# Kernel optimization log

Hardware: AMD Instinct MI355X
Metric: run time of the kernel (lower is better)

The kernel has to match this reference:

```python
import jax, jax.numpy as jnp
import numpy as np

B, N, IN, H, I, A, NA, NH = 4096, 8, 256, 256, 64, 64, 32, 256
VAR_FLOOR = 0.002
BN_EPS = 1e-5


def _lin(x, w, b):
    # torch Linear: x @ w.T + b, w: [out, in]
    return x @ w.T + b


def _bn_train(x, g, b):
    # BatchNorm1d in training mode: batch stats, biased variance
    mu = jnp.mean(x, axis=0)
    var = jnp.var(x, axis=0)
    return (x - mu) * jax.lax.rsqrt(var + BN_EPS) * g + b


def _intent_net(h_la, w1, b1, g, bbn, w2, b2):
    z = _lin(h_la, w1, b1)
    z = _bn_train(z, g, bbn)
    z = jax.nn.leaky_relu(z, 0.01)
    return _lin(z, w2, b2)


def setup_inputs() -> dict:
    key = jax.random.key(0)
    ks = jax.random.split(key, 30)
    s = 0.05
    d = {
        "inputs": jax.random.normal(ks[0], (B * N, IN), jnp.float32),
        "last_actions": jax.random.normal(ks[1], (B, N, NA), jnp.float32),
        "hidden_state": jax.random.normal(ks[2], (B * N, H), jnp.float32),
        "eps": jax.random.normal(ks[3], (B * N, I), jnp.float32),
        # fc1
        "fc1_w": jax.random.normal(ks[4], (H, IN), jnp.float32) * s,
        "fc1_b": jnp.zeros((H,), jnp.float32),
        # GRUCell (r,z,n gate order, torch layout)
        "gru_w_ih": jax.random.normal(ks[5], (3 * H, H), jnp.float32) * s,
        "gru_w_hh": jax.random.normal(ks[6], (3 * H, H), jnp.float32) * s,
        "gru_b_ih": jnp.zeros((3 * H,), jnp.float32),
        "gru_b_hh": jnp.zeros((3 * H,), jnp.float32),
        # intent_net: Linear(H+NA, NH) -> BN -> LeakyReLU -> Linear(NH, 2*I)
        "in1_w": jax.random.normal(ks[7], (NH, H + NA), jnp.float32) * s,
        "in1_b": jnp.zeros((NH,), jnp.float32),
        "bn_g": jnp.ones((NH,), jnp.float32),
        "bn_b": jnp.zeros((NH,), jnp.float32),
        "in2_w": jax.random.normal(ks[8], (2 * I, NH), jnp.float32) * s,
        "in2_b": jnp.zeros((2 * I,), jnp.float32),
        # attention projections
        "wq_w": jax.random.normal(ks[9], (A, I), jnp.float32) * s,
        "wq_b": jnp.zeros((A,), jnp.float32),
        "wk_w": jax.random.normal(ks[10], (A, I), jnp.float32) * s,
        "wk_b": jnp.zeros((A,), jnp.float32),
        "wv_w": jax.random.normal(ks[11], (A, I + H), jnp.float32) * s,
        "wv_b": jnp.zeros((A,), jnp.float32),
        # fc2
        "fc2_w": jax.random.normal(ks[12], (NA, H + A), jnp.float32) * s,
        "fc2_b": jnp.zeros((NA,), jnp.float32),
        "bs": B,
        "t": 1,
    }
    return d


def reference(inputs, last_actions, hidden_state, eps,
              fc1_w, fc1_b, gru_w_ih, gru_w_hh, gru_b_ih, gru_b_hh,
              in1_w, in1_b, bn_g, bn_b, in2_w, in2_b,
              wq_w, wq_b, wk_w, wk_b, wv_w, wv_b, fc2_w, fc2_b,
              bs, t):
    n = N
    x = jax.nn.relu(_lin(inputs, fc1_w, fc1_b))  # [bs*n, H]
    h_in = hidden_state.reshape(-1, H)
    # torch GRUCell
    gi = x @ gru_w_ih.T + gru_b_ih
    gh = h_in @ gru_w_hh.T + gru_b_hh
    i_r, i_z, i_n = jnp.split(gi, 3, axis=-1)
    h_r, h_z, h_n = jnp.split(gh, 3, axis=-1)
    r = jax.nn.sigmoid(i_r + h_r)
    z = jax.nn.sigmoid(i_z + h_z)
    nng = jnp.tanh(i_n + r * h_n)
    h = (1.0 - z) * nng + z * h_in  # [bs*n, H]

    la = last_actions.reshape(bs * n, NA)
    h_la = jnp.concatenate([h, la], axis=-1)
    ip = _intent_net(h_la, in1_w, in1_b, bn_g, bn_b, in2_w, in2_b)  # [bs*n, 2I]
    mean = ip[:, :I]
    std = jnp.maximum(jnp.exp(ip[:, I:]), VAR_FLOOR)
    intent = mean + eps * std  # reparameterized sample, [bs*n, I]

    q = _lin(intent, wq_w, wq_b).reshape(bs, n, A)  # query per agent i
    k = _lin(intent, wk_w, wk_b).reshape(bs, n, A)  # key per agent j
    scale = 1.0 / jnp.sqrt(jnp.float32(A))
    alpha = jnp.einsum('bia,bja->bij', q * scale, k)  # [bs, n, n]
    diag = jnp.eye(n, dtype=bool)
    alpha = jnp.where(diag[None], -1e9, alpha)
    alpha = jax.nn.softmax(alpha, axis=-1)

    v = _lin(jnp.concatenate([intent, h], axis=-1), wv_w, wv_b).reshape(bs, n, A)
    combined = jnp.einsum('bij,bja->bia', alpha, v).reshape(bs * n, A)

    local_Q = _lin(jnp.concatenate([h, combined], axis=-1), fc2_w, fc2_b).reshape(bs, n, NA)
    # final intent_embed: fresh intent_net output (no clamp/exp applied)
    intent_embed = _intent_net(h_la, in1_w, in1_b, bn_g, bn_b, in2_w, in2_b)
    return local_Q, h, intent, intent_embed
```

## Files before the change

### kernel.cpp

```cpp
#include <hip/hip_runtime.h>
#include <hip/hip_bf16.h>

#define BN_ 32768

using bf16 = __hip_bfloat16;
typedef __bf16 v8bf __attribute__((ext_vector_type(8)));
typedef unsigned short v8us __attribute__((ext_vector_type(8)));
typedef float v4f __attribute__((ext_vector_type(4)));

__device__ __forceinline__ float b2f(bf16 x) { return __bfloat162float(x); }
__device__ __forceinline__ bf16 f2b(float x) { return __float2bfloat16(x); }
__device__ __forceinline__ unsigned short f2bu(float x) {
  bf16 h = __float2bfloat16(x);
  return *reinterpret_cast<unsigned short*>(&h);
}
__device__ __forceinline__ float bu2f(unsigned short u) {
  union { unsigned int i; float f; } x;
  x.i = ((unsigned int)u) << 16;
  return x.f;
}
__device__ __forceinline__ void gl_lds16(const void* g, void* l) {
  __builtin_amdgcn_global_load_lds(
      (const __attribute__((address_space(1))) void*)g,
      (__attribute__((address_space(3))) void*)l, 16, 0, 0);
}
__device__ __forceinline__ float fsig(float x) { return 1.f / (1.f + __expf(-x)); }
__device__ __forceinline__ float ftanh(float x) {
  return 1.f - 2.f / (__expf(2.f * x) + 1.f);
}
template <int CF>
__device__ __forceinline__ void cstore(void* C, size_t off, float v) {
  if constexpr (CF) ((float*)C)[off] = v;
  else ((bf16*)C)[off] = f2b(v);
}
__device__ __forceinline__ int xcd_swz() {
  const int nbx = gridDim.x, nby = gridDim.y;
  const int f = blockIdx.y * nbx + blockIdx.x;
  const int nwg = nbx * nby;
  const int q = nwg >> 3, r = nwg & 7;
  const int xcd = f & 7, l = f >> 3;
  if (r == 0) return xcd * q + l;
  return (xcd < r ? xcd * (q + 1) : r * (q + 1) + (xcd - r) * q) + l;
}

template <int TM, int TN, int WR, int WC, int ACT, int A1M, int A2M, int KS, int KSB,
          int CF, int ATF, int STATS, int QKV>
__global__ __launch_bounds__(256) void gemm_bt(
    const void* __restrict__ A1, int lda1, const void* __restrict__ A2, int lda2,
    const bf16* __restrict__ B1, const bf16* __restrict__ B2, int ldb,
    const float* __restrict__ bias, void* C, int ldc, int K,
    const float* __restrict__ tsc, const float* __restrict__ tsh,
    float* __restrict__ PART, const float* __restrict__ pe,
    float* __restrict__ pit, unsigned short* __restrict__ pitb, void* C2) {
  constexpr int BK = 64;
  __shared__ __align__(16) unsigned short As[TM * BK];
  __shared__ __align__(16) unsigned short Bs[TN * BK];
  const int tid = threadIdx.x;
  const int wv = tid >> 6;
  const int lane = tid & 63;
  const int w = xcd_swz();
  const int bm = (w / gridDim.y) * TM;
  const int bn = (w % gridDim.y) * TN;

  constexpr int WM = TM / WR, WN = TN / WC;
  constexpr int FM = WM / 16, FN = WN / 16;
  const int wm0 = (wv % WR) * WM;
  const int wn0 = (wv / WR) * WN;

  v4f acc[FM][FN];
  const v4f vzero = {0.f, 0.f, 0.f, 0.f};
  for (int i = 0; i < FM; ++i)
    for (int j = 0; j < FN; ++j) acc[i][j] = vzero;

  const int lrow = lane >> 3;
  const int lcol = (lane & 7) * 8;
  const int mr = lane & 15;
  const int kq = (lane >> 4) * 8;

  for (int k0 = 0; k0 < K; k0 += BK) {
    {
      const bool useA1 = (KS == 0) || (k0 < KS);
      const void* Ap = useA1 ? A1 : A2;
      const int lda = useA1 ? lda1 : lda2;
      const int ka = useA1 ? k0 : k0 - KS;
      const bool f32 = useA1 ? (A1M == 1) : (A2M == 1);
      if (ATF && useA1) {
        const unsigned short* Ab = (const unsigned short*)Ap;
        const float4 s0 = *(const float4*)(tsc + ka + lcol);
        const float4 s1 = *(const float4*)(tsc + ka + lcol + 4);
        const float4 h0 = *(const float4*)(tsh + ka + lcol);
        const float4 h1 = *(const float4*)(tsh + ka + lcol + 4);
        const float sc[8] = {s0.x, s0.y, s0.z, s0.w, s1.x, s1.y, s1.z, s1.w};
        const float sh[8] = {h0.x, h0.y, h0.z, h0.w, h1.x, h1.y, h1.z, h1.w};
        for (int ch = wv; ch < TM / 8; ch += 4) {
          const unsigned short* s = Ab + (size_t)(bm + ch * 8 + lrow) * lda + ka + lcol;
          v8us zin = *(const v8us*)s;
          v8us d;
#pragma unroll
          for (int u = 0; u < 8; ++u) {
            float v = bu2f(zin[u]) * sc[u] + sh[u];
            d[u] = f2bu(v > 0.f ? v : 0.01f * v);
          }
          *(v8us*)(As + ch * 8 * BK + lane * 8) = d;
        }
      } else if (f32) {
        const float* Af = (const float*)Ap;
        for (int ch = wv; ch < TM / 8; ch += 4) {
          const float* s = Af + (size_t)(bm + ch * 8 + lrow) * lda + ka + lcol;
          float4 x0 = *(const float4*)s;
          float4 x1 = *(const float4*)(s + 4);
          v8us d;
          d[0]=f2bu(x0.x); d[1]=f2bu(x0.y); d[2]=f2bu(x0.z); d[3]=f2bu(x0.w);
          d[4]=f2bu(x1.x); d[5]=f2bu(x1.y); d[6]=f2bu(x1.z); d[7]=f2bu(x1.w);
          *(v8us*)(As + ch * 8 * BK + lane * 8) = d;
        }
      } else {
        const unsigned short* Ab = (const unsigned short*)Ap;
        for (int ch = wv; ch < TM / 8; ch += 4)
          gl_lds16(Ab + (size_t)(bm + ch * 8 + lrow) * lda + ka + lcol,
                   As + ch * 8 * BK);
      }
    }
    {
      const bool useB1 = (KSB == 0) || (k0 < KSB);
      const bf16* Bp = useB1 ? B1 : B2;
      const int kb = useB1 ? k0 : k0 - KSB;
      for (int ch = wv; ch < TN / 8; ch += 4)
        gl_lds16((const unsigned short*)Bp + (size_t)(bn + ch * 8 + lrow) * ldb + kb + lcol,
                 Bs + ch * 8 * BK);
    }
    __syncthreads();
#pragma unroll
    for (int kk = 0; kk < BK; kk += 32) {
      v8bf af[FM], bfr[FN];
#pragma unroll
      for (int i = 0; i < FM; ++i)
        af[i] = *(const v8bf*)(As + (wm0 + i * 16 + mr) * BK + kk + kq);
#pragma unroll
      for (int j = 0; j < FN; ++j)
        bfr[j] = *(const v8bf*)(Bs + (wn0 + j * 16 + mr) * BK + kk + kq);
#pragma unroll
      for (int i = 0; i < FM; ++i)
#pragma unroll
        for (int j = 0; j < FN; ++j)
          acc[i][j] = __builtin_amdgcn_mfma_f32_16x16x32_bf16(af[i], bfr[j],
                                                              acc[i][j], 0, 0, 0);
    }
    __syncthreads();
  }
  const int crow = (lane >> 4) * 4;

  if constexpr (ACT == 5) {
#pragma unroll
    for (int j = 0; j < 4; ++j) {
      const int gcol = bn + j * 16 + mr;
      const float bmn = bias[gcol];
      const float bsd = bias[gcol + 64];
#pragma unroll
      for (int r = 0; r < 4; ++r) {
        const int grow = bm + wm0 + crow + r;
        const float mean = acc[0][j][r] + bmn;
        const float lstd = acc[0][j + 4][r] + bsd;
        ((float*)C)[(size_t)grow * 128 + gcol] = mean;
        ((float*)C)[(size_t)grow * 128 + gcol + 64] = lstd;
        const float sd = fmaxf(__expf(lstd), 0.002f);
        const float iv = mean + pe[(size_t)grow * 64 + gcol] * sd;
        pit[(size_t)grow * 64 + gcol] = iv;
        pitb[(size_t)grow * 512 + gcol] = f2bu(iv);
      }
    }
  } else {
#pragma unroll
    for (int j = 0; j < FN; ++j) {
      const int gcol = bn + wn0 + j * 16 + mr;
      const float bv = bias[gcol];
      float ps = 0.f, pq = 0.f;
#pragma unroll
      for (int i = 0; i < FM; ++i) {
#pragma unroll
        for (int r = 0; r < 4; ++r) {
          const int grow = bm + wm0 + i * 16 + crow + r;
          float v = acc[i][j][r] + bv;
          if (ACT == 1) v = v > 0.f ? v : 0.f;
          if constexpr (QKV) {
            if (gcol < 128) ((bf16*)C)[(size_t)grow * 128 + gcol] = f2b(v);
            else ((bf16*)C2)[(size_t)grow * 64 + (gcol - 128)] = f2b(v);
          } else if constexpr (STATS) {
            const unsigned short d = f2bu(v);
            ((bf16*)C)[(size_t)grow * ldc + gcol] = *(const bf16*)&d;
            const float vr = bu2f(d);
            ps += vr; pq += vr * vr;
          } else {
            cstore<CF>(C, (size_t)grow * ldc + gcol, v);
          }
        }
      }
      if constexpr (STATS) {
        ps += __shfl_xor(ps, 16); ps += __shfl_xor(ps, 32);
        pq += __shfl_xor(pq, 16); pq += __shfl_xor(pq, 32);
        if (lane < 16) {
          const int slot = (gcol << 10) + ((bm >> 6) << 1) + (wv % WR);
          PART[slot] = ps;
          PART[262144 + slot] = pq;
        }
      }
    }
  }
}

__global__ __launch_bounds__(64) void bn_finalize2(
    const float* __restrict__ PART, const float* __restrict__ g,
    const float* __restrict__ b, float* __restrict__ stats) {
  const int col = blockIdx.x;
  const int lane = threadIdx.x;
  const float4* ps = (const float4*)(PART + (col << 10));
  const float4* pq = (const float4*)(PART + 262144 + (col << 10));
  float s = 0.f, q = 0.f;
#pragma unroll
  for (int u = 0; u < 4; ++u) {
    const float4 a = ps[lane * 4 + u];
    const float4 c = pq[lane * 4 + u];
    s += a.x + a.y + a.z + a.w;
    q += c.x + c.y + c.z + c.w;
  }
#pragma unroll
  for (int m = 1; m < 64; m <<= 1) {
    s += __shfl_xor(s, m);
    q += __shfl_xor(q, m);
  }
  if (lane == 0) {
    const float mean = s * (1.f / 32768.f);
    float var = q * (1.f / 32768.f) - mean * mean;
    var = fmaxf(var, 0.f);
    const float sc = g[col] * rsqrtf(var + 1e-5f);
    stats[512 + col] = sc;
    stats[768 + col] = b[col] - mean * sc;
  }
}

__global__ __launch_bounds__(256) void gru_fused(
    const bf16* __restrict__ X, const bf16* __restrict__ HB,
    const bf16* __restrict__ Win, const bf16* __restrict__ Whn,
    const float* __restrict__ FBp, const bf16* G1, unsigned short* HB2,
    float* __restrict__ Hout) {
  constexpr int BK = 64;
  __shared__ __align__(16) char smem[49152];
  unsigned short* AsX = (unsigned short*)smem;
  unsigned short* AsH = AsX + 4096;
  unsigned short* Bin = AsH + 4096;
  unsigned short* Bhn = Bin + 8192;
  float* Ein = (float*)smem;
  float* Ehn = Ein + 64 * 68;

  const int tid = threadIdx.x;
  const int wv = tid >> 6;
  const int lane = tid & 63;
  const int w = xcd_swz();
  const int bm = (w / gridDim.y) * 64;
  const int bn = (w % gridDim.y) * 128;
  const int wm0 = (wv & 1) * 32;
  const int wn0 = (wv >> 1) * 64;

  v4f ain[2][4], ahn[2][4];
  const v4f vzero = {0.f, 0.f, 0.f, 0.f};
  for (int i = 0; i < 2; ++i)
    for (int j = 0; j < 4; ++j) { ain[i][j] = vzero; ahn[i][j] = vzero; }

  const int lrow = lane >> 3;
  const int lcol = (lane & 7) * 8;
  const int mr = lane & 15;
  const int kq = (lane >> 4) * 8;

  for (int k0 = 0; k0 < 256; k0 += BK) {
    for (int ch = wv; ch < 8; ch += 4) {
      const size_t aoff = (size_t)(bm + ch * 8 + lrow) * 256 + k0 + lcol;
      gl_lds16((const unsigned short*)X + aoff, AsX + ch * 8 * BK);
      gl_lds16((const unsigned short*)HB + aoff, AsH + ch * 8 * BK);
    }
    for (int ch = wv; ch < 16; ch += 4) {
      const size_t boff = (size_t)(bn + ch * 8 + lrow) * 256 + k0 + lcol;
      gl_lds16((const unsigned short*)Win + boff, Bin + ch * 8 * BK);
      gl_lds16((const unsigned short*)Whn + boff, Bhn + ch * 8 * BK);
    }
    __syncthreads();
#pragma unroll
    for (int kk = 0; kk < BK; kk += 32) {
      v8bf ax[2], ah[2], bi[4], bh[4];
#pragma unroll
      for (int i = 0; i < 2; ++i) {
        ax[i] = *(const v8bf*)(AsX + (wm0 + i * 16 + mr) * BK + kk + kq);
        ah[i] = *(const v8bf*)(AsH + (wm0 + i * 16 + mr) * BK + kk + kq);
      }
#pragma unroll
      for (int j = 0; j < 4; ++j) {
        bi[j] = *(const v8bf*)(Bin + (wn0 + j * 16 + mr) * BK + kk + kq);
        bh[j] = *(const v8bf*)(Bhn + (wn0 + j * 16 + mr) * BK + kk + kq);
      }
#pragma unroll
      for (int i = 0; i < 2; ++i)
#pragma unroll
        for (int j = 0; j < 4; ++j) {
          ain[i][j] = __builtin_amdgcn_mfma_f32_16x16x32_bf16(ax[i], bi[j],
                                                              ain[i][j], 0, 0, 0);
          ahn[i][j] = __builtin_amdgcn_mfma_f32_16x16x32_bf16(ah[i], bh[j],
                                                              ahn[i][j], 0, 0, 0);
        }
    }
    __syncthreads();
  }

  const int crow = (lane >> 4) * 4;
  const int myhalf = wn0 >> 6;
  const int c4 = (tid & 15) * 4;
#pragma unroll
  for (int h = 0; h < 2; ++h) {
    ushort4 r4a[4], z4a[4], hp4a[4];
#pragma unroll
    for (int it = 0; it < 4; ++it) {
      const int grow = bm + (tid >> 4) + it * 16;
      const int gcol = bn + h * 64 + c4;
      const unsigned short* g1p = (const unsigned short*)G1 + (size_t)grow * 512 + gcol;
      r4a[it] = *(const ushort4*)g1p;
      z4a[it] = *(const ushort4*)(g1p + 256);
      hp4a[it] = *(const ushort4*)((const unsigned short*)HB + (size_t)grow * 256 + gcol);
    }
    __syncthreads();
    if (myhalf == h) {
#pragma unroll
      for (int i = 0; i < 2; ++i)
#pragma unroll
        for (int j = 0; j < 4; ++j)
#pragma unroll
          for (int r = 0; r < 4; ++r) {
            const int idx = (wm0 + i * 16 + crow + r) * 68 + j * 16 + mr;
            Ein[idx] = ain[i][j][r];
            Ehn[idx] = ahn[i][j][r];
          }
    }
    __syncthreads();
#pragma unroll
    for (int it = 0; it < 4; ++it) {
      const int row = (tid >> 4) + it * 16;
      const int grow = bm + row;
      const int gcol = bn + h * 64 + c4;
      const float4 ei = *(const float4*)(Ein + row * 68 + c4);
      const float4 eh = *(const float4*)(Ehn + row * 68 + c4);
      const float4 bin4 = *(const float4*)(FBp + 768 + gcol);
      const float4 bhn4 = *(const float4*)(FBp + 1024 + gcol);
      const float rv[4] = {bu2f(r4a[it].x), bu2f(r4a[it].y), bu2f(r4a[it].z), bu2f(r4a[it].w)};
      const float zv[4] = {bu2f(z4a[it].x), bu2f(z4a[it].y), bu2f(z4a[it].z), bu2f(z4a[it].w)};
      const float hpv[4] = {bu2f(hp4a[it].x), bu2f(hp4a[it].y), bu2f(hp4a[it].z), bu2f(hp4a[it].w)};
      const float eiv[4] = {ei.x, ei.y, ei.z, ei.w};
      const float ehv[4] = {eh.x, eh.y, eh.z, eh.w};
      const float biv[4] = {bin4.x, bin4.y, bin4.z, bin4.w};
      const float bhv[4] = {bhn4.x, bhn4.y, bhn4.z, bhn4.w};
      float vo[4];
#pragma unroll
      for (int u = 0; u < 4; ++u) {
        float rr = fsig(rv[u]);
        float zz = fsig(zv[u]);
        float nn = ftanh(eiv[u] + biv[u] + rr * (ehv[u] + bhv[u]));
        vo[u] = (1.f - zz) * nn + zz * hpv[u];
      }
      *(float4*)(Hout + (size_t)grow * 256 + gcol) =
          make_float4(vo[0], vo[1], vo[2], vo[3]);
      ushort4 hb2;
      hb2.x = f2bu(vo[0]); hb2.y = f2bu(vo[1]);
      hb2.z = f2bu(vo[2]); hb2.w = f2bu(vo[3]);
      *(ushort4*)(HB2 + (size_t)grow * 512 + gcol) = hb2;
    }
  }
}

__global__ void conv_all(
    const float* fc1_w, const float* w_ih, const float* w_hh, const float* in1_w,
    const float* in2_w, const float* wq_w, const float* wk_w, const float* wv_w,
    const float* fc2_w, const float* fc1_b, const float* b_ih, const float* b_hh,
    const float* in1_b, const float* in2_b, const float* wq_b, const float* wk_b,
    const float* wv_b, const float* fc2_b, const float* bn_g, const float* bn_b,
    bf16* __restrict__ WF, float* __restrict__ FB) {
  int idx = blockIdx.x * 256 + threadIdx.x;
  if (idx < 673792) {
    float v;
    if (idx < 65536) v = fc1_w[idx];
    else if (idx < 262144) v = w_ih[idx - 65536];
    else if (idx < 458752) v = w_hh[idx - 262144];
    else if (idx < 540672) {
      int j = idx - 458752, r = j / 320, c = j % 320;
      v = (c < 288) ? in1_w[r * 288 + c] : 0.f;
    } else if (idx < 573440) v = in2_w[idx - 540672];
    else if (idx < 602112) {
      v = 0.f;
    } else if (idx < 612352) v = fc2_w[idx - 602112];
    else {
      int j = idx - 612352, r = j / 320, c = j % 320;
      if (r < 128) v = (c < 64) ? (r < 64 ? wq_w[r * 64 + c]
                                          : wk_w[(r - 64) * 64 + c]) : 0.f;
      else v = wv_w[(size_t)(r - 128) * 320 + c];
    }
    WF[idx] = f2b(v);
  } else if (idx < 677376) {
    int j = idx - 673792;
    float v;
    if (j < 256) v = fc1_b[j];
    else if (j < 768) v = b_ih[j - 256] + b_hh[j - 256];
    else if (j < 1024) v = b_ih[512 + j - 768];
    else if (j < 1280) v = b_hh[512 + j - 1024];
    else if (j < 1536) v = in1_b[j - 1280];
    else if (j < 1664) v = in2_b[j - 1536];
    else if (j < 1792) { int c = j - 1664; v = (c < 64) ? wq_b[c] : wk_b[c - 64]; }
    else if (j < 1856) v = wv_b[j - 1792];
    else if (j < 1888) v = fc2_b[j - 1856];
    else if (j < 2144) v = bn_g[j - 1888];
    else if (j < 2400) v = bn_b[j - 2144];
    else v = 0.f;
    FB[j] = v;
  }
}

__global__ void pack_all(const float* __restrict__ h, bf16* __restrict__ hb,
                         const float* __restrict__ x, bf16* __restrict__ xb,
                         const float* __restrict__ la, bf16* __restrict__ lap) {
  const int bid = blockIdx.x;
  if (bid < 8192) {
    const float* s = bid < 4096 ? h : x;
    bf16* d = bid < 4096 ? hb : xb;
    const int i = (bid & 4095) * 256 + threadIdx.x;
    const float4 x0 = ((const float4*)s)[i * 2];
    const float4 x1 = ((const float4*)s)[i * 2 + 1];
    v8us o;
    o[0]=f2bu(x0.x); o[1]=f2bu(x0.y); o[2]=f2bu(x0.z); o[3]=f2bu(x0.w);
    o[4]=f2bu(x1.x); o[5]=f2bu(x1.y); o[6]=f2bu(x1.z); o[7]=f2bu(x1.w);
    ((v8us*)d)[i] = o;
  } else {
    const int i = (bid - 8192) * 256 + threadIdx.x;
    const int row = i >> 3, cg = i & 7;
    v8us o;
    if (cg < 4) {
      const float4 a = *(const float4*)(la + (size_t)row * 32 + cg * 8);
      const float4 b = *(const float4*)(la + (size_t)row * 32 + cg * 8 + 4);
      o[0]=f2bu(a.x); o[1]=f2bu(a.y); o[2]=f2bu(a.z); o[3]=f2bu(a.w);
      o[4]=f2bu(b.x); o[5]=f2bu(b.y); o[6]=f2bu(b.z); o[7]=f2bu(b.w);
    } else {
      for (int u = 0; u < 8; ++u) o[u] = 0;
    }
    ((v8us*)lap)[i] = o;
  }
}

__global__ __launch_bounds__(256) void attn(const bf16* __restrict__ QK,
                                            const bf16* __restrict__ Vv,
                                            bf16* __restrict__ comb) {
  __shared__ float q[4][8][65], k[4][8][65], v[4][8][65];
  __shared__ float al[4][8][8];
  const int wv = threadIdx.x >> 6, t = threadIdx.x & 63;
  const int b = blockIdx.x * 4 + wv;
  const size_t rb = (size_t)b * 8;
  const unsigned short* qkb = (const unsigned short*)QK + rb * 128;
#pragma unroll
  for (int p = 0; p < 2; ++p) {
    const int e = t * 8 + p * 512;
    const int row = e >> 7, col = e & 127;
    v8us d = *(const v8us*)(qkb + row * 128 + col);
    if (col < 64) {
#pragma unroll
      for (int u = 0; u < 8; ++u) q[wv][row][col + u] = bu2f(d[u]);
    } else {
#pragma unroll
      for (int u = 0; u < 8; ++u) k[wv][row][col - 64 + u] = bu2f(d[u]);
    }
  }
  {
    const int e = t * 8;
    const int row = e >> 6, col = e & 63;
    v8us d = *(const v8us*)((const unsigned short*)Vv + rb * 64 + row * 64 + col);
#pragma unroll
    for (int u = 0; u < 8; ++u) v[wv][row][col + u] = bu2f(d[u]);
  }
  __syncthreads();
  const int i = t >> 3, j = t & 7;
  float s = 0.f;
#pragma unroll
  for (int a = 0; a < 64; ++a) s += q[wv][i][a] * k[wv][j][a];
  s *= 0.125f;
  if (i == j) s = -1e9f;
  float m = s;
  m = fmaxf(m, __shfl_xor(m, 1, 8));
  m = fmaxf(m, __shfl_xor(m, 2, 8));
  m = fmaxf(m, __shfl_xor(m, 4, 8));
  float e = __expf(s - m);
  float sum = e;
  sum += __shfl_xor(sum, 1, 8);
  sum += __shfl_xor(sum, 2, 8);
  sum += __shfl_xor(sum, 4, 8);
  al[wv][i][j] = e / sum;
  __syncthreads();
  const int a0 = (t & 7) * 8;
  v8us o8;
#pragma unroll
  for (int u = 0; u < 8; ++u) {
    float o = 0.f;
#pragma unroll
    for (int jj = 0; jj < 8; ++jj) o += al[wv][i][jj] * v[wv][jj][a0 + u];
    o8[u] = f2bu(o);
  }
  *(v8us*)((unsigned short*)comb + (rb + i) * 64 + a0) = o8;
}

extern "C" void kernel_launch(void* const* d_in, const int* in_sizes, int n_in,
                              void* d_out, int out_size, void* d_ws, size_t ws_size,
                              hipStream_t stream) {
  (void)in_sizes; (void)n_in; (void)out_size; (void)ws_size;
  const float* inputs = (const float*)d_in[0];
  const float* last_actions = (const float*)d_in[1];
  const float* hidden = (const float*)d_in[2];
  const float* eps = (const float*)d_in[3];

  float* out = (float*)d_out;
  float* out_lq = out;
  float* out_h = out + 1048576;
  float* out_it = out + 9437184;
  float* out_ie = out + 11534336;

  bf16* HB = (bf16*)(out + 11534336);
  bf16* XB = (bf16*)(out + 1048576);
  bf16* LAP = (bf16*)out_lq;
  float* PART = out + 9437184;

  char* ws = (char*)d_ws;
  bf16* X    = (bf16*)(ws + 0);
  bf16* G1   = (bf16*)(ws + 16777216);
  unsigned short* HB2 = (unsigned short*)(ws + 16777216);
  unsigned short* ITB = (unsigned short*)(ws + 16777216) + 256;
  bf16* Z1   = (bf16*)(ws + 0);
  bf16* QK   = (bf16*)(ws + 0);
  bf16* V    = (bf16*)(ws + 8388608);
  bf16* COMB = (bf16*)(ws + 12582912);
  float* FB  = (float*)(ws + 50331648);
  bf16*  WF  = (bf16*)(ws + 50348032);
  float* stats = FB + 2560;

  conv_all<<<2646, 256, 0, stream>>>(
      (const float*)d_in[4], (const float*)d_in[6], (const float*)d_in[7],
      (const float*)d_in[10], (const float*)d_in[14], (const float*)d_in[16],
      (const float*)d_in[18], (const float*)d_in[20], (const float*)d_in[22],
      (const float*)d_in[5], (const float*)d_in[8], (const float*)d_in[9],
      (const float*)d_in[11], (const float*)d_in[15], (const float*)d_in[17],
      (const float*)d_in[19], (const float*)d_in[21], (const float*)d_in[23],
      (const float*)d_in[12], (const float*)d_in[13], WF, FB);

  pack_all<<<9216, 256, 0, stream>>>(hidden, HB, inputs, XB, last_actions, LAP);

  gemm_bt<64, 128, 2, 2, 1, 0, 0, 0, 0, 0, 0, 0, 0><<<dim3(512, 2), 256, 0, stream>>>(
      XB, 256, nullptr, 0, WF + 0, nullptr, 256, FB + 0, X, 256, 256,
      nullptr, nullptr, nullptr, nullptr, nullptr, nullptr, nullptr);
  gemm_bt<64, 128, 2, 2, 0, 0, 0, 256, 256, 0, 0, 0, 0><<<dim3(512, 4), 256, 0, stream>>>(
      X, 256, HB, 256, WF + 65536, WF + 262144, 256, FB + 256, G1, 512, 512,
      nullptr, nullptr, nullptr, nullptr, nullptr, nullptr, nullptr);
  gru_fused<<<dim3(512, 2), 256, 0, stream>>>(
      X, HB, WF + 65536 + 512 * 256, WF + 262144 + 512 * 256, FB, G1, HB2, out_h);

  gemm_bt<64, 128, 2, 2, 0, 0, 0, 256, 0, 0, 0, 1, 0><<<dim3(512, 2), 256, 0, stream>>>(
      HB2, 512, LAP, 64, WF + 458752, nullptr, 320, FB + 1280, Z1, 256, 320,
      nullptr, nullptr, PART, nullptr, nullptr, nullptr, nullptr);
  bn_finalize2<<<256, 64, 0, stream>>>(PART, FB + 1888, FB + 2144, stats);
  gemm_bt<64, 128, 4, 1, 5, 0, 0, 0, 0, 1, 1, 0, 0><<<dim3(512, 1), 256, 0, stream>>>(
      Z1, 256, nullptr, 0, WF + 540672, nullptr, 256, FB + 1536, out_ie, 128, 256,
      stats + 512, stats + 768, nullptr, eps, out_it, ITB, nullptr);
  gemm_bt<64, 192, 2, 2, 0, 0, 0, 64, 0, 0, 0, 0, 1><<<dim3(512, 1), 256, 0, stream>>>(
      ITB, 512, HB2, 512, WF + 612352, nullptr, 320, FB + 1664, QK, 128, 320,
      nullptr, nullptr, nullptr, nullptr, nullptr, nullptr, V);
  attn<<<1024, 256, 0, stream>>>(QK, V, COMB);
  gemm_bt<64, 32, 4, 1, 0, 0, 0, 256, 0, 1, 0, 0, 0><<<dim3(512, 1), 256, 0, stream>>>(
      HB2, 512, COMB, 64, WF + 602112, nullptr, 320, FB + 1856, out_lq, 32, 320,
      nullptr, nullptr, nullptr, nullptr, nullptr, nullptr, nullptr);
}
```

Baseline: 314.0 us.

## Fuse full GRU gate GEMMs and nonlinearity into one kernel, drop G1 buffer

The separate r/z gate GEMM, which wrote a bf16 G1 intermediate, is merged into a single GRU kernel. Each block computes all three gates from both the input and hidden projections for a 64x64 output tile and applies the GRU update in registers. This removes one launch and the G1 write and read round trip, and HB2/ITB are repacked into dense buffers with new strides. In exchange each block loads six weight tiles per K step, and the X/H tiles are reloaded across four column blocks, which raises register and LDS pressure.

```diff
diff --git a/kernel.cpp b/kernel.cpp
--- a/kernel.cpp
+++ b/kernel.cpp
@@ -166,7 +166,7 @@
         const float sd = fmaxf(__expf(lstd), 0.002f);
         const float iv = mean + pe[(size_t)grow * 64 + gcol] * sd;
         pit[(size_t)grow * 64 + gcol] = iv;
-        pitb[(size_t)grow * 512 + gcol] = f2bu(iv);
+        pitb[(size_t)grow * 64 + gcol] = f2bu(iv);
       }
     }
   } else {
@@ -238,33 +238,32 @@
   }
 }
 
-__global__ __launch_bounds__(256) void gru_fused(
+__global__ __launch_bounds__(256) void gru_full(
     const bf16* __restrict__ X, const bf16* __restrict__ HB,
-    const bf16* __restrict__ Win, const bf16* __restrict__ Whn,
-    const float* __restrict__ FBp, const bf16* G1, unsigned short* HB2,
+    const bf16* __restrict__ Wih, const bf16* __restrict__ Whh,
+    const float* __restrict__ FBp, unsigned short* __restrict__ HB2,
     float* __restrict__ Hout) {
   constexpr int BK = 64;
-  __shared__ __align__(16) char smem[49152];
-  unsigned short* AsX = (unsigned short*)smem;
-  unsigned short* AsH = AsX + 4096;
-  unsigned short* Bin = AsH + 4096;
-  unsigned short* Bhn = Bin + 8192;
+  __shared__ __align__(16) unsigned short smem[32768];
   float* Ein = (float*)smem;
-  float* Ehn = Ein + 64 * 68;
 
   const int tid = threadIdx.x;
   const int wv = tid >> 6;
   const int lane = tid & 63;
   const int w = xcd_swz();
-  const int bm = (w / gridDim.y) * 64;
-  const int bn = (w % gridDim.y) * 128;
+  const int bm = (w >> 2) * 64;
+  const int cb = w & 3;
   const int wm0 = (wv & 1) * 32;
-  const int wn0 = (wv >> 1) * 64;
-
-  v4f ain[2][4], ahn[2][4];
+  const int wn0 = (wv >> 1) * 32;
+
+  v4f ax_[3][2][2], ah_[3][2][2];
   const v4f vzero = {0.f, 0.f, 0.f, 0.f};
-  for (int i = 0; i < 2; ++i)
-    for (int j = 0; j < 4; ++j) { ain[i][j] = vzero; ahn[i][j] = vzero; }
+#pragma unroll
+  for (int m = 0; m < 3; ++m)
+#pragma unroll
+    for (int i = 0; i < 2; ++i)
+#pragma unroll
+      for (int j = 0; j < 2; ++j) { ax_[m][i][j] = vzero; ah_[m][i][j] = vzero; }
 
   const int lrow = lane >> 3;
   const int lcol = (lane & 7) * 8;
@@ -272,103 +271,103 @@
   const int kq = (lane >> 4) * 8;
 
   for (int k0 = 0; k0 < 256; k0 += BK) {
-    for (int ch = wv; ch < 8; ch += 4) {
-      const size_t aoff = (size_t)(bm + ch * 8 + lrow) * 256 + k0 + lcol;
-      gl_lds16((const unsigned short*)X + aoff, AsX + ch * 8 * BK);
-      gl_lds16((const unsigned short*)HB + aoff, AsH + ch * 8 * BK);
-    }
-    for (int ch = wv; ch < 16; ch += 4) {
-      const size_t boff = (size_t)(bn + ch * 8 + lrow) * 256 + k0 + lcol;
-      gl_lds16((const unsigned short*)Win + boff, Bin + ch * 8 * BK);
-      gl_lds16((const unsigned short*)Whn + boff, Bhn + ch * 8 * BK);
+    for (int job = wv; job < 64; job += 4) {
+      const int t = job >> 3, c = job & 7;
+      const int row8 = c * 8 + lrow;
+      const unsigned short* src;
+      if (t == 0)
+        src = (const unsigned short*)X + (size_t)(bm + row8) * 256 + k0 + lcol;
+      else if (t == 1)
+        src = (const unsigned short*)HB + (size_t)(bm + row8) * 256 + k0 + lcol;
+      else if (t < 5)
+        src = (const unsigned short*)Wih +
+              (size_t)((t - 2) * 256 + cb * 64 + row8) * 256 + k0 + lcol;
+      else
+        src = (const unsigned short*)Whh +
+              (size_t)((t - 5) * 256 + cb * 64 + row8) * 256 + k0 + lcol;
+      gl_lds16(src, smem + t * 4096 + c * 512);
     }
     __syncthreads();
 #pragma unroll
     for (int kk = 0; kk < BK; kk += 32) {
-      v8bf ax[2], ah[2], bi[4], bh[4];
+      v8bf a0[2], a1[2];
 #pragma unroll
       for (int i = 0; i < 2; ++i) {
-        ax[i] = *(const v8bf*)(AsX + (wm0 + i * 16 + mr) * BK + kk + kq);
-        ah[i] = *(const v8bf*)(AsH + (wm0 + i * 16 + mr) * BK + kk + kq);
-      }
-#pragma unroll
-      for (int j = 0; j < 4; ++j) {
-        bi[j] = *(const v8bf*)(Bin + (wn0 + j * 16 + mr) * BK + kk + kq);
-        bh[j] = *(const v8bf*)(Bhn + (wn0 + j * 16 + mr) * BK + kk + kq);
-      }
-#pragma unroll
-      for (int i = 0; i < 2; ++i)
-#pragma unroll
-        for (int j = 0; j < 4; ++j) {
-          ain[i][j] = __builtin_amdgcn_mfma_f32_16x16x32_bf16(ax[i], bi[j],
-                                                              ain[i][j], 0, 0, 0);
-          ahn[i][j] = __builtin_amdgcn_mfma_f32_16x16x32_bf16(ah[i], bh[j],
-                                                              ahn[i][j], 0, 0, 0);
+        a0[i] = *(const v8bf*)(smem + (wm0 + i * 16 + mr) * 64 + kk + kq);
+        a1[i] = *(const v8bf*)(smem + 4096 + (wm0 + i * 16 + mr) * 64 + kk + kq);
+      }
+#pragma unroll
+      for (int m = 0; m < 3; ++m) {
+        v8bf b0[2], b1[2];
+#pragma unroll
+        for (int j = 0; j < 2; ++j) {
+          b0[j] = *(const v8bf*)(smem + (2 + m) * 4096 + (wn0 + j * 16 + mr) * 64 + kk + kq);
+          b1[j] = *(const v8bf*)(smem + (5 + m) * 4096 + (wn0 + j * 16 + mr) * 64 + kk + kq);
         }
+#pragma unroll
+        for (int i = 0; i < 2; ++i)
+#pragma unroll
+          for (int j = 0; j < 2; ++j) {
+            ax_[m][i][j] = __builtin_amdgcn_mfma_f32_16x16x32_bf16(
+                a0[i], b0[j], ax_[m][i][j], 0, 0, 0);
+            ah_[m][i][j] = __builtin_amdgcn_mfma_f32_16x16x32_bf16(
+                a1[i], b1[j], ah_[m][i][j], 0, 0, 0);
+          }
+      }
     }
     __syncthreads();
   }
 
   const int crow = (lane >> 4) * 4;
-  const int myhalf = wn0 >> 6;
-  const int c4 = (tid & 15) * 4;
-#pragma unroll
-  for (int h = 0; h < 2; ++h) {
-    ushort4 r4a[4], z4a[4], hp4a[4];
-#pragma unroll
-    for (int it = 0; it < 4; ++it) {
-      const int grow = bm + (tid >> 4) + it * 16;
-      const int gcol = bn + h * 64 + c4;
-      const unsigned short* g1p = (const unsigned short*)G1 + (size_t)grow * 512 + gcol;
-      r4a[it] = *(const ushort4*)g1p;
-      z4a[it] = *(const ushort4*)(g1p + 256);
-      hp4a[it] = *(const ushort4*)((const unsigned short*)HB + (size_t)grow * 256 + gcol);
-    }
-    __syncthreads();
-    if (myhalf == h) {
-#pragma unroll
-      for (int i = 0; i < 2; ++i)
-#pragma unroll
-        for (int j = 0; j < 4; ++j)
-#pragma unroll
-          for (int r = 0; r < 4; ++r) {
-            const int idx = (wm0 + i * 16 + crow + r) * 68 + j * 16 + mr;
-            Ein[idx] = ain[i][j][r];
-            Ehn[idx] = ahn[i][j][r];
-          }
-    }
-    __syncthreads();
-#pragma unroll
-    for (int it = 0; it < 4; ++it) {
-      const int row = (tid >> 4) + it * 16;
-      const int grow = bm + row;
-      const int gcol = bn + h * 64 + c4;
-      const float4 ei = *(const float4*)(Ein + row * 68 + c4);
-      const float4 eh = *(const float4*)(Ehn + row * 68 + c4);
-      const float4 bin4 = *(const float4*)(FBp + 768 + gcol);
-      const float4 bhn4 = *(const float4*)(FBp + 1024 + gcol);
-      const float rv[4] = {bu2f(r4a[it].x), bu2f(r4a[it].y), bu2f(r4a[it].z), bu2f(r4a[it].w)};
-      const float zv[4] = {bu2f(z4a[it].x), bu2f(z4a[it].y), bu2f(z4a[it].z), bu2f(z4a[it].w)};
-      const float hpv[4] = {bu2f(hp4a[it].x), bu2f(hp4a[it].y), bu2f(hp4a[it].z), bu2f(hp4a[it].w)};
-      const float eiv[4] = {ei.x, ei.y, ei.z, ei.w};
-      const float ehv[4] = {eh.x, eh.y, eh.z, eh.w};
-      const float biv[4] = {bin4.x, bin4.y, bin4.z, bin4.w};
-      const float bhv[4] = {bhn4.x, bhn4.y, bhn4.z, bhn4.w};
-      float vo[4];
-#pragma unroll
-      for (int u = 0; u < 4; ++u) {
-        float rr = fsig(rv[u]);
-        float zz = fsig(zv[u]);
-        float nn = ftanh(eiv[u] + biv[u] + rr * (ehv[u] + bhv[u]));
-        vo[u] = (1.f - zz) * nn + zz * hpv[u];
-      }
-      *(float4*)(Hout + (size_t)grow * 256 + gcol) =
-          make_float4(vo[0], vo[1], vo[2], vo[3]);
-      ushort4 hb2;
-      hb2.x = f2bu(vo[0]); hb2.y = f2bu(vo[1]);
-      hb2.z = f2bu(vo[2]); hb2.w = f2bu(vo[3]);
-      *(ushort4*)(HB2 + (size_t)grow * 512 + gcol) = hb2;
-    }
+  unsigned short hp[2][2][4];
+#pragma unroll
+  for (int i = 0; i < 2; ++i)
+#pragma unroll
+    for (int j = 0; j < 2; ++j)
+#pragma unroll
+      for (int r = 0; r < 4; ++r)
+        hp[i][j][r] = ((const unsigned short*)HB)
+            [(size_t)(bm + wm0 + i * 16 + crow + r) * 256 + cb * 64 + wn0 + j * 16 + mr];
+#pragma unroll
+  for (int j = 0; j < 2; ++j) {
+    const int gc = cb * 64 + wn0 + j * 16 + mr;
+    const float br = FBp[256 + gc];
+    const float bz = FBp[512 + gc];
+    const float bin = FBp[768 + gc];
+    const float bhn = FBp[1024 + gc];
+#pragma unroll
+    for (int i = 0; i < 2; ++i)
+#pragma unroll
+      for (int r = 0; r < 4; ++r) {
+        const float rr = fsig(ax_[0][i][j][r] + ah_[0][i][j][r] + br);
+        const float zz = fsig(ax_[1][i][j][r] + ah_[1][i][j][r] + bz);
+        const float nn = ftanh(ax_[2][i][j][r] + bin + rr * (ah_[2][i][j][r] + bhn));
+        const float hv = (1.f - zz) * nn + zz * bu2f(hp[i][j][r]);
+        Ein[(wm0 + i * 16 + crow + r) * 68 + wn0 + j * 16 + mr] = hv;
+      }
+  }
+  __syncthreads();
+  {
+    const int orow = tid >> 2;
+    const int oq = (tid & 3) * 16;
+    float tmp[16];
+#pragma unroll
+    for (int u = 0; u < 4; ++u) {
+      const float4 f = *(const float4*)(Ein + orow * 68 + oq + u * 4);
+      tmp[u * 4 + 0] = f.x; tmp[u * 4 + 1] = f.y;
+      tmp[u * 4 + 2] = f.z; tmp[u * 4 + 3] = f.w;
+    }
+    float* ho = Hout + (size_t)(bm + orow) * 256 + cb * 64 + oq;
+#pragma unroll
+    for (int u = 0; u < 4; ++u)
+      ((float4*)ho)[u] = make_float4(tmp[u * 4], tmp[u * 4 + 1], tmp[u * 4 + 2],
+                                     tmp[u * 4 + 3]);
+    v8us hb0, hb1;
+#pragma unroll
+    for (int u = 0; u < 8; ++u) { hb0[u] = f2bu(tmp[u]); hb1[u] = f2bu(tmp[8 + u]); }
+    unsigned short* hbo = HB2 + (size_t)(bm + orow) * 256 + cb * 64 + oq;
+    *(v8us*)hbo = hb0;
+    *(v8us*)(hbo + 8) = hb1;
   }
 }
 
@@ -529,9 +528,8 @@
 
   char* ws = (char*)d_ws;
   bf16* X    = (bf16*)(ws + 0);
-  bf16* G1   = (bf16*)(ws + 16777216);
   unsigned short* HB2 = (unsigned short*)(ws + 16777216);
-  unsigned short* ITB = (unsigned short*)(ws + 16777216) + 256;
+  unsigned short* ITB = (unsigned short*)(ws + 33554432);
   bf16* Z1   = (bf16*)(ws + 0);
   bf16* QK   = (bf16*)(ws + 0);
   bf16* V    = (bf16*)(ws + 8388608);
@@ -554,24 +552,21 @@
   gemm_bt<64, 128, 2, 2, 1, 0, 0, 0, 0, 0, 0, 0, 0><<<dim3(512, 2), 256, 0, stream>>>(
       XB, 256, nullptr, 0, WF + 0, nullptr, 256, FB + 0, X, 256, 256,
       nullptr, nullptr, nullptr, nullptr, nullptr, nullptr, nullptr);
-  gemm_bt<64, 128, 2, 2, 0, 0, 0, 256, 256, 0, 0, 0, 0><<<dim3(512, 4), 256, 0, stream>>>(
-      X, 256, HB, 256, WF + 65536, WF + 262144, 256, FB + 256, G1, 512, 512,
-      nullptr, nullptr, nullptr, nullptr, nullptr, nullptr, nullptr);
-  gru_fused<<<dim3(512, 2), 256, 0, stream>>>(
-      X, HB, WF + 65536 + 512 * 256, WF + 262144 + 512 * 256, FB, G1, HB2, out_h);
+  gru_full<<<2048, 256, 0, stream>>>(
+      X, HB, WF + 65536, WF + 262144, FB, HB2, out_h);
 
   gemm_bt<64, 128, 2, 2, 0, 0, 0, 256, 0, 0, 0, 1, 0><<<dim3(512, 2), 256, 0, stream>>>(
-      HB2, 512, LAP, 64, WF + 458752, nullptr, 320, FB + 1280, Z1, 256, 320,
+      HB2, 256, LAP, 64, WF + 458752, nullptr, 320, FB + 1280, Z1, 256, 320,
       nullptr, nullptr, PART, nullptr, nullptr, nullptr, nullptr);
   bn_finalize2<<<256, 64, 0, stream>>>(PART, FB + 1888, FB + 2144, stats);
   gemm_bt<64, 128, 4, 1, 5, 0, 0, 0, 0, 1, 1, 0, 0><<<dim3(512, 1), 256, 0, stream>>>(
       Z1, 256, nullptr, 0, WF + 540672, nullptr, 256, FB + 1536, out_ie, 128, 256,
       stats + 512, stats + 768, nullptr, eps, out_it, ITB, nullptr);
   gemm_bt<64, 192, 2, 2, 0, 0, 0, 64, 0, 0, 0, 0, 1><<<dim3(512, 1), 256, 0, stream>>>(
-      ITB, 512, HB2, 512, WF + 612352, nullptr, 320, FB + 1664, QK, 128, 320,
+      ITB, 64, HB2, 256, WF + 612352, nullptr, 320, FB + 1664, QK, 128, 320,
       nullptr, nullptr, nullptr, nullptr, nullptr, nullptr, V);
   attn<<<1024, 256, 0, stream>>>(QK, V, COMB);
   gemm_bt<64, 32, 4, 1, 0, 0, 0, 256, 0, 1, 0, 0, 0><<<dim3(512, 1), 256, 0, stream>>>(
-      HB2, 512, COMB, 64, WF + 602112, nullptr, 320, FB + 1856, out_lq, 32, 320,
+      HB2, 256, COMB, 64, WF + 602112, nullptr, 320, FB + 1856, out_lq, 32, 320,
       nullptr, nullptr, nullptr, nullptr, nullptr, nullptr, nullptr);
 }
```

After: 384.9 us. 22.6% more time.
